# Performance work log

Hardware: AMD Instinct MI355X
Metric: run time of the kernel (lower is better)

The kernel has to match this reference:

```python
import math
import jax, jax.numpy as jnp
import numpy as np

D_MODEL = 1024
NUM_HEADS = 16
D_K = D_MODEL // NUM_HEADS
RANK = 16
B, L = 2, 2048


def setup_inputs() -> dict:
    key = jax.random.key(0)
    ks = jax.random.split(key, 10)
    w_scale = 0.02  # keep activations well-scaled like trained linears
    return {
        "x_q": jax.random.normal(ks[0], (B, L, D_MODEL), jnp.float32),
        "x_kv": jax.random.normal(ks[1], (B, L, D_MODEL), jnp.float32),
        "Wq": jax.random.normal(ks[2], (D_MODEL, D_MODEL), jnp.float32) * w_scale,
        "bq": jnp.zeros((D_MODEL,), jnp.float32),
        "Wk": jax.random.normal(ks[3], (D_MODEL, D_MODEL), jnp.float32) * w_scale,
        "bk": jnp.zeros((D_MODEL,), jnp.float32),
        "Wv": jax.random.normal(ks[4], (D_MODEL, D_MODEL), jnp.float32) * w_scale,
        "bv": jnp.zeros((D_MODEL,), jnp.float32),
        "Wo": jax.random.normal(ks[5], (D_MODEL, D_MODEL), jnp.float32) * w_scale,
        "bo": jnp.zeros((D_MODEL,), jnp.float32),
        "U_bil": jax.random.normal(ks[6], (NUM_HEADS, D_K, RANK), jnp.float32) * 0.02,
        "V_bil": jax.random.normal(ks[7], (NUM_HEADS, D_K, RANK), jnp.float32) * 0.02,
        "padding_mask": jnp.zeros((B, L), bool),  # True = padded KV position
    }


def reference(x_q, x_kv, Wq, bq, Wk, bk, Wv, bv, Wo, bo, U_bil, V_bil, padding_mask):
    b, l, _ = x_q.shape
    # torch nn.Linear: y = x @ W.T + b
    Q = (x_q @ Wq.T + bq).reshape(b, l, NUM_HEADS, D_K).transpose(0, 2, 1, 3)  # [B,H,L,dk]
    K = (x_kv @ Wk.T + bk).reshape(b, l, NUM_HEADS, D_K).transpose(0, 2, 1, 3)
    V = (x_kv @ Wv.T + bv).reshape(b, l, NUM_HEADS, D_K).transpose(0, 2, 1, 3)
    # low-rank bilinear projections: [B,H,L,rank]
    Q_proj = jnp.einsum("bhld,hdr->bhlr", Q, U_bil)
    K_proj = jnp.einsum("bhld,hdr->bhlr", K, V_bil)
    scores = jnp.einsum("bhqr,bhkr->bhqk", Q_proj, K_proj) / math.sqrt(RANK)  # [B,H,L,L]
    scores = jnp.where(padding_mask[:, None, None, :], jnp.float32(-10000.0), scores)
    attn = jax.nn.softmax(scores, axis=-1)  # dropout is identity in eval mode
    ctx = jnp.einsum("bhqk,bhkd->bhqd", attn, V)
    ctx = ctx.transpose(0, 2, 1, 3).reshape(b, l, D_MODEL)
    return ctx @ Wo.T + bo
```

## Files before the change

kernel.cpp:

```cpp
#include <hip/hip_runtime.h>
#include <hip/hip_bf16.h>

#define DM   1024
#define NH   16
#define DK   64
#define RK   16
#define BB   2
#define LL   2048
#define TT   (BB*LL)
#define HRK  256
#define NSPL 2


typedef float f4   __attribute__((ext_vector_type(4)));
typedef float f16v __attribute__((ext_vector_type(16)));
typedef short s8v  __attribute__((ext_vector_type(8)));
typedef unsigned int u2v __attribute__((ext_vector_type(2)));
typedef unsigned int u4v __attribute__((ext_vector_type(4)));

static __device__ __forceinline__ unsigned short f2b(float f) {
  __hip_bfloat16 h = __float2bfloat16(f);
  unsigned short u;
  __builtin_memcpy(&u, &h, 2);
  return u;
}
static __device__ __forceinline__ float b2f(unsigned short u) {
  __hip_bfloat16 h;
  __builtin_memcpy(&h, &u, 2);
  return __bfloat162float(h);
}

static __device__ __forceinline__ void gld_lds16(const void* g, void* l) {
  __builtin_amdgcn_global_load_lds(
      (const __attribute__((address_space(1))) unsigned int*)g,
      (__attribute__((address_space(3))) unsigned int*)l, 16, 0, 0);
}

__global__ __launch_bounds__(256) void cast_all(
    const float* __restrict__ s0, unsigned short* __restrict__ d0, int n0,
    const float* __restrict__ s1, unsigned short* __restrict__ d1, int n1,
    const float* __restrict__ s2, unsigned short* __restrict__ d2, int n2,
    const float* __restrict__ s3, unsigned short* __restrict__ d3, int n3) {
  const float* s; unsigned short* d; int n;
  switch (blockIdx.y) {
    case 0:  s = s0; d = d0; n = n0; break;
    case 1:  s = s1; d = d1; n = n1; break;
    case 2:  s = s2; d = d2; n = n2; break;
    default: s = s3; d = d3; n = n3; break;
  }
  for (int i = blockIdx.x*256 + threadIdx.x; i < n; i += gridDim.x*256) {
    const float4 v = ((const float4*)s)[i];
    ushort4 o;
    o.x = f2b(v.x); o.y = f2b(v.y); o.z = f2b(v.z); o.w = f2b(v.w);
    ((ushort4*)d)[i] = o;
  }
}

__global__ __launch_bounds__(256) void fuse_w(
    const float* __restrict__ Wq, const float* __restrict__ Wk,
    const float* __restrict__ Uq, const float* __restrict__ Uk,
    unsigned short* __restrict__ Aq, unsigned short* __restrict__ Ak) {
  const float* W = blockIdx.z ? Wk : Wq;
  const float* U = blockIdx.z ? Uk : Uq;
  unsigned short* At = blockIdx.z ? Ak : Aq;
  __shared__ float Us[64][16];
  __shared__ float Ws[4][64];
  const int i0 = blockIdx.x * 64;
  const int h  = blockIdx.y;
  const int tid = threadIdx.x;
  const int il = tid & 63, rr = tid >> 6;
  for (int t = tid; t < 64*16; t += 256)
    Us[t >> 4][t & 15] = U[(size_t)(h*DK + (t >> 4))*RK + (t & 15)];
  float acc[4] = {};
  for (int d0 = 0; d0 < DK; d0 += 4) {
    __syncthreads();
    Ws[rr][il] = W[(size_t)(h*DK + d0 + rr)*DM + i0 + il];
    __syncthreads();
#pragma unroll
    for (int dd = 0; dd < 4; ++dd) {
      const float w = Ws[dd][il];
#pragma unroll
      for (int j = 0; j < 4; ++j)
        acc[j] += w * Us[d0 + dd][rr*4 + j];
    }
  }
#pragma unroll
  for (int j = 0; j < 4; ++j)
    At[(size_t)(h*RK + rr*4 + j)*DM + i0 + il] = f2b(acc[j]);
}

__global__ void bias2(const float* __restrict__ bq, const float* __restrict__ bk,
                      const float* __restrict__ Uq, const float* __restrict__ Uk,
                      float* __restrict__ bpq, float* __restrict__ bpk) {
  const int t = threadIdx.x;
  const float* b = (t < 256) ? bq : bk;
  const float* U = (t < 256) ? Uq : Uk;
  float* bp = (t < 256) ? bpq : bpk;
  const int hr = t & 255, h = hr >> 4, r = hr & 15;
  float acc = 0.f;
  for (int d = 0; d < DK; ++d)
    acc += b[h*DK + d] * U[(size_t)(h*DK + d)*RK + r];
  bp[hr] = acc;
}

__global__ __launch_bounds__(256) void vsum_k(
    const unsigned short* __restrict__ Vt, float* __restrict__ Vsum) {
  const int h = blockIdx.x, b = blockIdx.y;
  const int d = threadIdx.x >> 2, part = threadIdx.x & 3;
  const unsigned short* row = Vt + ((size_t)b*DM + h*DK + d)*LL + part*512;
  float s = 0.f;
  for (int i = 0; i < 512; i += 8) {
    const s8v v = *(const s8v*)&row[i];
#pragma unroll
    for (int j = 0; j < 8; ++j) s += b2f((unsigned short)v[j]);
  }
  s += __shfl_xor(s, 1);
  s += __shfl_xor(s, 2);
  if (part == 0) Vsum[((size_t)b*NH + h)*DK + d] = s;
}

template<int N_, int MODE>
__global__ __launch_bounds__(256) void gemm64(
    const unsigned short* __restrict__ A0, const unsigned short* __restrict__ A1,
    const unsigned short* __restrict__ B0, const unsigned short* __restrict__ B1,
    const float* __restrict__ bi0, const float* __restrict__ bi1,
    void* __restrict__ C0, void* __restrict__ C1) {
  const unsigned short* Ag = blockIdx.z ? A1 : A0;
  const unsigned short* Bg = blockIdx.z ? B1 : B0;
  const float* bias = blockIdx.z ? bi1 : bi0;
  void* Cgv = blockIdx.z ? C1 : C0;
  __shared__ __align__(16) unsigned short Xs[64*32];
  __shared__ __align__(16) unsigned short Bs[128*32];
  const int t0 = blockIdx.x * 64, n0 = blockIdx.y * 128;
  const int tid = threadIdx.x, wave = tid >> 6, lane = tid & 63;
  const int quad = lane >> 4, l15 = lane & 15;
  const int nh = wave * 32;
  const int ar = tid >> 2, ac = (tid & 3) * 8;

  const f4 z = {0.f, 0.f, 0.f, 0.f};
  f4 acc[4][2];
#pragma unroll
  for (int a = 0; a < 4; ++a) { acc[a][0] = z; acc[a][1] = z; }

  for (int k0 = 0; k0 < DM; k0 += 32) {
    __syncthreads();
    gld_lds16(&Ag[(size_t)(t0 + ar)*DM + k0 + ac],       &Xs[wave*512]);
    gld_lds16(&Bg[(size_t)(n0 + ar)*DM + k0 + ac],       &Bs[wave*512]);
    gld_lds16(&Bg[(size_t)(n0 + 64 + ar)*DM + k0 + ac],  &Bs[2048 + wave*512]);
    __syncthreads();

    s8v af[4], bf[2];
#pragma unroll
    for (int ms = 0; ms < 4; ++ms)
      af[ms] = *(const s8v*)&Xs[(ms*16 + l15)*32 + quad*8];
#pragma unroll
    for (int ns = 0; ns < 2; ++ns)
      bf[ns] = *(const s8v*)&Bs[(nh + ns*16 + l15)*32 + quad*8];
#pragma unroll
    for (int ms = 0; ms < 4; ++ms)
#pragma unroll
      for (int ns = 0; ns < 2; ++ns)
        acc[ms][ns] = __builtin_amdgcn_mfma_f32_16x16x32_bf16(
            af[ms], bf[ns], acc[ms][ns], 0, 0, 0);
  }

#pragma unroll
  for (int ms = 0; ms < 4; ++ms) {
    const int tb = t0 + ms*16 + quad*4;
#pragma unroll
    for (int ns = 0; ns < 2; ++ns) {
      const int o = n0 + nh + ns*16 + l15;
      const float bv = bias[o];
      f4 a = acc[ms][ns];
      if (MODE == 0) {
        float* C = (float*)Cgv;
#pragma unroll
        for (int rg = 0; rg < 4; ++rg)
          C[(size_t)(tb + rg)*N_ + o] = a[rg] + bv;
      } else if (MODE == 1) {
        unsigned short* C = (unsigned short*)Cgv;
#pragma unroll
        for (int rg = 0; rg < 4; ++rg) {
          const int tt = tb + rg;
          C[(((size_t)(tt >> 11)*NH + (o >> 4))*LL + (tt & 2047))*RK + (o & 15)]
              = f2b(a[rg] + bv);
        }
      } else {
        unsigned short* C = (unsigned short*)Cgv;
        const int bb = tb >> 11, l = tb & 2047;
        ushort4 pk;
        pk.x = f2b(a[0] + bv); pk.y = f2b(a[1] + bv);
        pk.z = f2b(a[2] + bv); pk.w = f2b(a[3] + bv);
        *(ushort4*)&C[((size_t)bb*DM + o)*LL + l] = pk;
      }
    }
  }
}

template<bool MASKED>
static __device__ __forceinline__ void softmax_pack(
    const f16v& s0, const f16v& s1, const unsigned long long mb, const int hi,
    float& den, unsigned int (&Pd)[2][4][2]) {
#pragma unroll
  for (int nt = 0; nt < 2; ++nt) {
    const f16v& sv = nt ? s1 : s0;
#pragma unroll
    for (int r = 0; r < 4; ++r) {
      float ep[4];
#pragma unroll
      for (int j = 0; j < 4; ++j) {
        float em = __expf(sv[r*4 + j] * 0.25f);
        if (MASKED) {
          const int kloc = nt*32 + j + 8*r + 4*hi;
          if ((mb >> kloc) & 1ull) em = 0.f;
        }
        den += em;
        ep[j] = em - 1.f;
      }
      asm("v_cvt_pk_bf16_f32 %0, %1, %2"
          : "=v"(Pd[nt][r][0]) : "v"(ep[0]), "v"(ep[1]));
      asm("v_cvt_pk_bf16_f32 %0, %1, %2"
          : "=v"(Pd[nt][r][1]) : "v"(ep[2]), "v"(ep[3]));
    }
  }
}

__global__ __launch_bounds__(256) void attention_v8(
    const unsigned short* __restrict__ Qp, const unsigned short* __restrict__ Kp,
    const unsigned short* __restrict__ Vt,
    const unsigned char* __restrict__ msk,
    unsigned short* __restrict__ P, float* __restrict__ denP) {
  __shared__ __align__(16) unsigned short Ks[2][2][64][8];
  __shared__ __align__(16) unsigned short Vs[2][8][64][8];
  const int q0 = blockIdx.x * 128, h = blockIdx.y;
  const int b = blockIdx.z & (BB - 1), ksp = blockIdx.z >> 1;
  const int kbeg = ksp * (LL / NSPL);
  const int NT = (LL / NSPL) / 64;
  const int tid = threadIdx.x, w = tid >> 6, lane = tid & 63;
  const int l31 = lane & 31, hi = lane >> 5;

  const s8v qfrag = *(const s8v*)&Qp[
      (((size_t)b*NH + h)*LL + q0 + w*32 + l31)*RK + hi*8];

  const int sr = tid >> 2, sp = tid & 3;
  const unsigned short* __restrict__ Vrow =
      Vt + ((size_t)b*DM + h*DK + sr)*LL + kbeg;
  const unsigned short* __restrict__ Kbase =
      Kp + (((size_t)b*NH + h)*LL + kbeg + sr)*RK + sp*4;
  const unsigned char*  __restrict__ Mrow = msk + (size_t)b*LL + kbeg + lane;

  u2v kpre; s8v vpre0, vpre1;
  unsigned char mcur, mnext;

  kpre  = *(const u2v*)&Kbase[0];
  vpre0 = *(const s8v*)&Vrow[sp*16];
  vpre1 = *(const s8v*)&Vrow[sp*16 + 8];
  mcur  = Mrow[0];
  *(u2v*)&Ks[0][sp>>1][sr][(sp&1)*4] = kpre;
  *(s8v*)&Vs[0][sp*2][sr][0]   = vpre0;
  *(s8v*)&Vs[0][sp*2+1][sr][0] = vpre1;
  kpre  = *(const u2v*)&Kbase[(size_t)64*RK];
  vpre0 = *(const s8v*)&Vrow[64 + sp*16];
  vpre1 = *(const s8v*)&Vrow[64 + sp*16 + 8];
  mnext = Mrow[64];
  __syncthreads();

  f16v acc0, acc1, z16;
#pragma unroll
  for (int i = 0; i < 16; ++i) { acc0[i] = 0.f; acc1[i] = 0.f; z16[i] = 0.f; }
  float den = 0.f;

  for (int t = 0; t < NT; ++t) {
    const int cur = t & 1;
    const unsigned long long mb = __ballot(mcur != 0);

    const s8v kf0 = *(const s8v*)&Ks[cur][hi][l31][0];
    const s8v kf1 = *(const s8v*)&Ks[cur][hi][32 + l31][0];

    const f16v s0 = __builtin_amdgcn_mfma_f32_32x32x16_bf16(kf0, qfrag, z16, 0, 0, 0);
    const f16v s1 = __builtin_amdgcn_mfma_f32_32x32x16_bf16(kf1, qfrag, z16, 0, 0, 0);

    unsigned int Pd[2][4][2];
    if (__builtin_expect(mb != 0ull, 0))
      softmax_pack<true >(s0, s1, mb, hi, den, Pd);
    else
      softmax_pack<false>(s0, s1, mb, hi, den, Pd);

#pragma unroll
    for (int kc = 0; kc < 4; ++kc) {
      const int nt = kc >> 1, a = (kc & 1)*2;
      const u2v r0 = __builtin_amdgcn_permlane32_swap(
          Pd[nt][a][0], Pd[nt][a+1][0], false, false);
      const u2v r1 = __builtin_amdgcn_permlane32_swap(
          Pd[nt][a][1], Pd[nt][a+1][1], false, false);
      u4v efi;
      efi[0] = r0[0];
      efi[1] = r1[0];
      efi[2] = r0[1];
      efi[3] = r1[1];
      const s8v ef = __builtin_bit_cast(s8v, efi);
      const s8v vf0 = *(const s8v*)&Vs[cur][kc*2 + hi][l31][0];
      const s8v vf1 = *(const s8v*)&Vs[cur][kc*2 + hi][32 + l31][0];
      acc0 = __builtin_amdgcn_mfma_f32_32x32x16_bf16(ef, vf0, acc0, 0, 0, 0);
      acc1 = __builtin_amdgcn_mfma_f32_32x32x16_bf16(ef, vf1, acc1, 0, 0, 0);
    }

    if (t + 1 < NT) {
      *(u2v*)&Ks[cur^1][sp>>1][sr][(sp&1)*4] = kpre;
      *(s8v*)&Vs[cur^1][sp*2][sr][0]   = vpre0;
      *(s8v*)&Vs[cur^1][sp*2+1][sr][0] = vpre1;
      const int tn = (t + 2 < NT) ? t + 2 : NT - 1;
      kpre  = *(const u2v*)&Kbase[(size_t)tn*64*RK];
      vpre0 = *(const s8v*)&Vrow[tn*64 + sp*16];
      vpre1 = *(const s8v*)&Vrow[tn*64 + sp*16 + 8];
      mcur  = mnext;
      mnext = Mrow[tn*64];
    }
    __syncthreads();
  }

  den += __shfl_xor(den, 32);
  if (hi == 0)
    denP[(((size_t)ksp*BB + b)*NH + h)*LL + q0 + w*32 + l31] = den;

#pragma unroll
  for (int rg = 0; rg < 16; ++rg) {
    const int qr = (rg & 3) + 8*(rg >> 2) + 4*hi;
    const size_t base = 2*(((size_t)(b*LL + q0 + w*32 + qr))*DM + h*DK) + ksp;
    P[base + 2*l31]        = f2b(acc0[rg]);
    P[base + 2*(32 + l31)] = f2b(acc1[rg]);
  }
}

__global__ __launch_bounds__(256) void reduce_k(
    const unsigned int* __restrict__ P, const float* __restrict__ Vsum,
    const float* __restrict__ denP, unsigned short* __restrict__ ctxb) {
  const size_t j0 = ((size_t)blockIdx.x*256 + threadIdx.x)*4;
  const int t  = (int)(j0 >> 10);
  const int dm = (int)(j0 & 1023);
  const int b = t >> 11, l = t & 2047;
  const int h = dm >> 6, d = dm & 63;
  const float dn =
      denP[((size_t)b*NH + h)*LL + l] +
      denP[(((size_t)BB + b)*NH + h)*LL + l];
  const float inv = 1.f / fmaxf(dn, 1e-30f);
  const f4 vs = *(const f4*)&Vsum[((size_t)b*NH + h)*DK + d];
  const u4v p = *(const u4v*)&P[j0];
  ushort4 pk;
  float c0 = (vs[0] + b2f((unsigned short)(p[0] & 0xffff))
                    + b2f((unsigned short)(p[0] >> 16))) * inv;
  float c1 = (vs[1] + b2f((unsigned short)(p[1] & 0xffff))
                    + b2f((unsigned short)(p[1] >> 16))) * inv;
  float c2 = (vs[2] + b2f((unsigned short)(p[2] & 0xffff))
                    + b2f((unsigned short)(p[2] >> 16))) * inv;
  float c3 = (vs[3] + b2f((unsigned short)(p[3] & 0xffff))
                    + b2f((unsigned short)(p[3] >> 16))) * inv;
  pk.x = f2b(c0); pk.y = f2b(c1); pk.z = f2b(c2); pk.w = f2b(c3);
  *(ushort4*)&ctxb[j0] = pk;
}

extern "C" void kernel_launch(void* const* d_in, const int* in_sizes, int n_in,
                              void* d_out, int out_size, void* d_ws, size_t ws_size,
                              hipStream_t stream) {
  (void)in_sizes; (void)n_in; (void)out_size; (void)ws_size;
  const float* x_q   = (const float*)d_in[0];
  const float* x_kv  = (const float*)d_in[1];
  const float* Wq    = (const float*)d_in[2];
  const float* bq    = (const float*)d_in[3];
  const float* Wk    = (const float*)d_in[4];
  const float* bk    = (const float*)d_in[5];
  const float* Wv    = (const float*)d_in[6];
  const float* bv    = (const float*)d_in[7];
  const float* Wo    = (const float*)d_in[8];
  const float* bo    = (const float*)d_in[9];
  const float* U_bil = (const float*)d_in[10];
  const float* V_bil = (const float*)d_in[11];
  const unsigned char* pmask = (const unsigned char*)d_in[12];
  float* out = (float*)d_out;

  char* w = (char*)d_ws;
  unsigned short* xq_b  = (unsigned short*)(w);
  unsigned short* xkv_b = (unsigned short*)(w +  8388608);
  unsigned short* Wv_b  = (unsigned short*)(w + 16777216);
  unsigned short* Wo_b  = (unsigned short*)(w + 18874368);
  unsigned short* Atq   = (unsigned short*)(w + 20971520);
  unsigned short* Atk   = (unsigned short*)(w + 21495808);
  float*          bpq   = (float*)(w + 22020096);
  float*          bpk   = (float*)(w + 22021120);
  unsigned short* Qp    = (unsigned short*)(w + 22022144);
  unsigned short* Kp    = (unsigned short*)(w + 24119296);
  unsigned short* Vt    = (unsigned short*)(w + 26216448);
  float*          Vsum  = (float*)(w + 34605056);
  float*          denP  = (float*)(w + 34613248);
  unsigned short* Pbuf  = (unsigned short*)w;
  unsigned short* ctxb  = Vt;

  cast_all<<<dim3(1024, 4), 256, 0, stream>>>(
      x_q, xq_b, TT*DM/4, x_kv, xkv_b, TT*DM/4,
      Wv, Wv_b, DM*DM/4,  Wo, Wo_b, DM*DM/4);
  fuse_w<<<dim3(DM/64, NH, 2), 256, 0, stream>>>(Wq, Wk, U_bil, V_bil, Atq, Atk);
  bias2<<<1, 512, 0, stream>>>(bq, bk, U_bil, V_bil, bpq, bpk);
  gemm64<HRK, 1><<<dim3(64, 2, 2), 256, 0, stream>>>(
      xq_b, xkv_b, Atq, Atk, bpq, bpk, Qp, Kp);
  gemm64<DM, 2><<<dim3(64, 8, 1), 256, 0, stream>>>(
      xkv_b, xkv_b, Wv_b, Wv_b, bv, bv, Vt, Vt);
  vsum_k<<<dim3(NH, BB), 256, 0, stream>>>(Vt, Vsum);
  attention_v8<<<dim3(LL/128, NH, BB*NSPL), 256, 0, stream>>>(
      Qp, Kp, Vt, pmask, Pbuf, denP);
  reduce_k<<<dim3(TT*DM/1024), 256, 0, stream>>>(
      (const unsigned int*)w, Vsum, denP, ctxb);
  gemm64<DM, 0><<<dim3(64, 8, 1), 256, 0, stream>>>(
      ctxb, ctxb, Wo_b, Wo_b, bo, bo, out, out);
}
```

Baseline: 251.5 us.

## Use 128x128 GEMM tiles for V and output projections, split V-sum reduction

```diff
diff --git a/kernel.cpp b/kernel.cpp
--- a/kernel.cpp
+++ b/kernel.cpp
@@ -104,19 +104,20 @@
 }
 
 __global__ __launch_bounds__(256) void vsum_k(
-    const unsigned short* __restrict__ Vt, float* __restrict__ Vsum) {
-  const int h = blockIdx.x, b = blockIdx.y;
+    const unsigned short* __restrict__ Vt, float* __restrict__ Vsum4) {
+  const int h = blockIdx.x, b = blockIdx.y, c = blockIdx.z;
   const int d = threadIdx.x >> 2, part = threadIdx.x & 3;
-  const unsigned short* row = Vt + ((size_t)b*DM + h*DK + d)*LL + part*512;
+  const unsigned short* row =
+      Vt + ((size_t)b*DM + h*DK + d)*LL + c*512 + part*128;
   float s = 0.f;
-  for (int i = 0; i < 512; i += 8) {
+  for (int i = 0; i < 128; i += 8) {
     const s8v v = *(const s8v*)&row[i];
 #pragma unroll
     for (int j = 0; j < 8; ++j) s += b2f((unsigned short)v[j]);
   }
   s += __shfl_xor(s, 1);
   s += __shfl_xor(s, 2);
-  if (part == 0) Vsum[((size_t)b*NH + h)*DK + d] = s;
+  if (part == 0) Vsum4[(((size_t)c*BB + b)*NH + h)*DK + d] = s;
 }
 
 template<int N_, int MODE>
@@ -172,12 +173,7 @@
       const int o = n0 + nh + ns*16 + l15;
       const float bv = bias[o];
       f4 a = acc[ms][ns];
-      if (MODE == 0) {
-        float* C = (float*)Cgv;
-#pragma unroll
-        for (int rg = 0; rg < 4; ++rg)
-          C[(size_t)(tb + rg)*N_ + o] = a[rg] + bv;
-      } else if (MODE == 1) {
+      if (MODE == 1) {
         unsigned short* C = (unsigned short*)Cgv;
 #pragma unroll
         for (int rg = 0; rg < 4; ++rg) {
@@ -185,6 +181,70 @@
           C[(((size_t)(tt >> 11)*NH + (o >> 4))*LL + (tt & 2047))*RK + (o & 15)]
               = f2b(a[rg] + bv);
         }
+      } else {
+        float* C = (float*)Cgv;
+#pragma unroll
+        for (int rg = 0; rg < 4; ++rg)
+          C[(size_t)(tb + rg)*N_ + o] = a[rg] + bv;
+      }
+    }
+  }
+}
+
+template<int N_, int MODE>
+__global__ __launch_bounds__(256) void gemm128(
+    const unsigned short* __restrict__ Ag, const unsigned short* __restrict__ Bg,
+    const float* __restrict__ bias, void* __restrict__ Cgv) {
+  __shared__ __align__(16) unsigned short As[128*32];
+  __shared__ __align__(16) unsigned short Bs[128*32];
+  const int t0 = blockIdx.x * 128, n0 = blockIdx.y * 128;
+  const int tid = threadIdx.x, wave = tid >> 6, lane = tid & 63;
+  const int quad = lane >> 4, l15 = lane & 15;
+  const int ar = tid >> 2, ac = (tid & 3) * 8;
+
+  const f4 z = {0.f, 0.f, 0.f, 0.f};
+  f4 acc[2][8];
+#pragma unroll
+  for (int m = 0; m < 2; ++m)
+#pragma unroll
+    for (int n = 0; n < 8; ++n) acc[m][n] = z;
+
+  for (int k0 = 0; k0 < DM; k0 += 32) {
+    __syncthreads();
+    gld_lds16(&Ag[(size_t)(t0 + ar)*DM + k0 + ac],       &As[wave*512]);
+    gld_lds16(&Ag[(size_t)(t0 + 64 + ar)*DM + k0 + ac],  &As[2048 + wave*512]);
+    gld_lds16(&Bg[(size_t)(n0 + ar)*DM + k0 + ac],       &Bs[wave*512]);
+    gld_lds16(&Bg[(size_t)(n0 + 64 + ar)*DM + k0 + ac],  &Bs[2048 + wave*512]);
+    __syncthreads();
+
+    s8v af[2], bf[8];
+#pragma unroll
+    for (int ms = 0; ms < 2; ++ms)
+      af[ms] = *(const s8v*)&As[(wave*32 + ms*16 + l15)*32 + quad*8];
+#pragma unroll
+    for (int ns = 0; ns < 8; ++ns)
+      bf[ns] = *(const s8v*)&Bs[(ns*16 + l15)*32 + quad*8];
+#pragma unroll
+    for (int ms = 0; ms < 2; ++ms)
+#pragma unroll
+      for (int ns = 0; ns < 8; ++ns)
+        acc[ms][ns] = __builtin_amdgcn_mfma_f32_16x16x32_bf16(
+            af[ms], bf[ns], acc[ms][ns], 0, 0, 0);
+  }
+
+#pragma unroll
+  for (int ms = 0; ms < 2; ++ms) {
+    const int tb = t0 + wave*32 + ms*16 + quad*4;
+#pragma unroll
+    for (int ns = 0; ns < 8; ++ns) {
+      const int o = n0 + ns*16 + l15;
+      const float bv = bias[o];
+      f4 a = acc[ms][ns];
+      if (MODE == 0) {
+        float* C = (float*)Cgv;
+#pragma unroll
+        for (int rg = 0; rg < 4; ++rg)
+          C[(size_t)(tb + rg)*N_ + o] = a[rg] + bv;
       } else {
         unsigned short* C = (unsigned short*)Cgv;
         const int bb = tb >> 11, l = tb & 2047;
@@ -333,7 +393,7 @@
 }
 
 __global__ __launch_bounds__(256) void reduce_k(
-    const unsigned int* __restrict__ P, const float* __restrict__ Vsum,
+    const unsigned int* __restrict__ P, const float* __restrict__ Vsum4,
     const float* __restrict__ denP, unsigned short* __restrict__ ctxb) {
   const size_t j0 = ((size_t)blockIdx.x*256 + threadIdx.x)*4;
   const int t  = (int)(j0 >> 10);
@@ -344,7 +404,12 @@
       denP[((size_t)b*NH + h)*LL + l] +
       denP[(((size_t)BB + b)*NH + h)*LL + l];
   const float inv = 1.f / fmaxf(dn, 1e-30f);
-  const f4 vs = *(const f4*)&Vsum[((size_t)b*NH + h)*DK + d];
+  f4 vs = {0.f, 0.f, 0.f, 0.f};
+#pragma unroll
+  for (int c = 0; c < 4; ++c) {
+    const f4 v = *(const f4*)&Vsum4[(((size_t)c*BB + b)*NH + h)*DK + d];
+    vs[0] += v[0]; vs[1] += v[1]; vs[2] += v[2]; vs[3] += v[3];
+  }
   const u4v p = *(const u4v*)&P[j0];
   ushort4 pk;
   float c0 = (vs[0] + b2f((unsigned short)(p[0] & 0xffff))
@@ -390,8 +455,8 @@
   unsigned short* Qp    = (unsigned short*)(w + 22022144);
   unsigned short* Kp    = (unsigned short*)(w + 24119296);
   unsigned short* Vt    = (unsigned short*)(w + 26216448);
-  float*          Vsum  = (float*)(w + 34605056);
   float*          denP  = (float*)(w + 34613248);
+  float*          Vsum4 = (float*)(w + 35137536);
   unsigned short* Pbuf  = (unsigned short*)w;
   unsigned short* ctxb  = Vt;
 
@@ -402,13 +467,11 @@
   bias2<<<1, 512, 0, stream>>>(bq, bk, U_bil, V_bil, bpq, bpk);
   gemm64<HRK, 1><<<dim3(64, 2, 2), 256, 0, stream>>>(
       xq_b, xkv_b, Atq, Atk, bpq, bpk, Qp, Kp);
-  gemm64<DM, 2><<<dim3(64, 8, 1), 256, 0, stream>>>(
-      xkv_b, xkv_b, Wv_b, Wv_b, bv, bv, Vt, Vt);
-  vsum_k<<<dim3(NH, BB), 256, 0, stream>>>(Vt, Vsum);
+  gemm128<DM, 2><<<dim3(32, 8), 256, 0, stream>>>(xkv_b, Wv_b, bv, Vt);
+  vsum_k<<<dim3(NH, BB, 4), 256, 0, stream>>>(Vt, Vsum4);
   attention_v8<<<dim3(LL/128, NH, BB*NSPL), 256, 0, stream>>>(
       Qp, Kp, Vt, pmask, Pbuf, denP);
   reduce_k<<<dim3(TT*DM/1024), 256, 0, stream>>>(
-      (const unsigned int*)w, Vsum, denP, ctxb);
-  gemm64<DM, 0><<<dim3(64, 8, 1), 256, 0, stream>>>(
-      ctxb, ctxb, Wo_b, Wo_b, bo, bo, out, out);
-}
+      (const unsigned int*)w, Vsum4, denP, ctxb);
+  gemm128<DM, 0><<<dim3(32, 8), 256, 0, stream>>>(ctxb, Wo_b, bo, out);
+}
```

Measured after the change: 255.5 us. About the same (+1.6%).
